# Kernel optimization log

Measured on AMD Instinct MI355X. Metric: run time of the kernel, lower is better.

## Reference

```python
import jax, jax.numpy as jnp
import numpy as np

WINDOW_SIZE = 11
CHANNELS = 3

def _gaussian_window(window_size=WINDOW_SIZE, channels=CHANNELS, sigma=1.5):
    x = np.arange(window_size, dtype=np.float32)
    g = np.exp(-((x - window_size // 2) ** 2) / (2.0 * sigma ** 2))
    g = g / g.sum()
    w2d = np.outer(g, g).astype(np.float32)  # [K,K]
    # depthwise kernel [C, 1, K, K] (OIHW with feature_group_count=C)
    return jnp.asarray(np.broadcast_to(w2d, (channels, 1, window_size, window_size)).copy())

def _depthwise_conv(x, window):
    # x: [B,C,H,W], window: [C,1,K,K]; SAME padding via explicit pad = K//2
    pad = window.shape[-1] // 2
    return jax.lax.conv_general_dilated(
        x, window,
        window_strides=(1, 1),
        padding=[(pad, pad), (pad, pad)],
        dimension_numbers=('NCHW', 'OIHW', 'NCHW'),
        feature_group_count=x.shape[1])

def setup_inputs() -> dict:
    key = jax.random.key(0)
    k1, k2 = jax.random.split(key)
    B, C, H, W = 16, 3, 512, 512
    img1 = jax.random.uniform(k1, (B, C, H, W), dtype=jnp.float32)
    img2 = jax.random.uniform(k2, (B, C, H, W), dtype=jnp.float32)
    window = _gaussian_window()
    return {"img1": img1, "img2": img2, "window": window}

def reference(img1, img2, window):
    eps = 1e-6
    img1 = jnp.clip(img1, eps, 1.0 - eps)
    img2 = jnp.clip(img2, eps, 1.0 - eps)

    mu1 = _depthwise_conv(img1, window)
    mu2 = _depthwise_conv(img2, window)
    mu1_sq = mu1 * mu1
    mu2_sq = mu2 * mu2
    mu1_mu2 = mu1 * mu2

    sigma1_sq = _depthwise_conv(img1 * img1, window) - mu1_sq
    sigma2_sq = _depthwise_conv(img2 * img2, window) - mu2_sq
    sigma12 = _depthwise_conv(img1 * img2, window) - mu1_mu2

    C1 = 0.01 ** 2
    C2 = 0.03 ** 2
    ssim_map = ((2.0 * mu1_mu2 + C1) * (2.0 * sigma12 + C2)) / (
        (mu1_sq + mu2_sq + C1) * (sigma1_sq + sigma2_sq + C2))
    return 1.0 - jnp.mean(ssim_map)
```

## Files before the change

kernel.cpp:

```cpp
#include <hip/hip_runtime.h>

typedef _Float16 f16;
typedef __fp16 fp16x2 __attribute__((ext_vector_type(2)));
typedef _Float16 half4 __attribute__((ext_vector_type(4)));
typedef _Float16 half8 __attribute__((ext_vector_type(8)));
typedef float floatx16 __attribute__((ext_vector_type(16)));

#define FSTR 44
#define XSTR 180
#define WTOT (32 * XSTR)

union H8 { half8 v; half4 h[2]; fp16x2 p[4]; unsigned u[4]; };
union H4 { half4 v; fp16x2 p[2]; };


__device__ __forceinline__ void load_tile(
    const float* __restrict__ img1, const float* __restrict__ img2, size_t base,
    int row, int rowcap, int x0, int q, float4 ra[3][2], float4 rb[3][2], unsigned mk[3])
{
    int rowc = min(max(min(row, rowcap), 0), 511);
    bool rok = (row >= 0) && (row <= 511);
    const float* r1 = img1 + base + (size_t)rowc * 512;
    const float* r2 = img2 + base + (size_t)rowc * 512;
    #pragma unroll
    for (int ch = 0; ch < 3; ++ch) {
        int cb  = x0 - 8 + 16 * ch + 8 * q;
        int cbc = min(max(cb, 0), 504);
        mk[ch] = (cb == cbc && rok) ? 0xFFFFFFFFu : 0u;
        ra[ch][0] = *(const float4*)(r1 + cbc);
        ra[ch][1] = *(const float4*)(r1 + cbc + 4);
        rb[ch][0] = *(const float4*)(r2 + cbc);
        rb[ch][1] = *(const float4*)(r2 + cbc + 4);
    }
}

__device__ __forceinline__ void compute_acct(
    const float4 ra[3][2], const float4 rb[3][2], const unsigned mk[3],
    const half8 band1[3], floatx16 acc[4])
{
    #pragma unroll
    for (int ch = 0; ch < 3; ++ch) {
        H8 F0, F1, F2, F3;
        #pragma unroll
        for (int h = 0; h < 2; ++h) {
            const float as[4] = {ra[ch][h].x, ra[ch][h].y, ra[ch][h].z, ra[ch][h].w};
            const float bs[4] = {rb[ch][h].x, rb[ch][h].y, rb[ch][h].z, rb[ch][h].w};
            #pragma unroll
            for (int t = 0; t < 2; ++t) {
                float a0 = as[2*t], a1 = as[2*t+1];
                float b0 = bs[2*t], b1 = bs[2*t+1];
                int jj = 2 * h + t;
                F0.p[jj] = __builtin_amdgcn_cvt_pkrtz(a0, a1);
                F1.p[jj] = __builtin_amdgcn_cvt_pkrtz(b0, b1);
                F2.p[jj] = __builtin_amdgcn_cvt_pkrtz(a0*a0 + b0*b0, a1*a1 + b1*b1);
                F3.p[jj] = __builtin_amdgcn_cvt_pkrtz(a0*b0, a1*b1);
            }
        }
        unsigned m = mk[ch];
        #pragma unroll
        for (int i = 0; i < 4; ++i) { F0.u[i] &= m; F1.u[i] &= m; F2.u[i] &= m; F3.u[i] &= m; }
        acc[0] = __builtin_amdgcn_mfma_f32_32x32x16_f16(F0.v, band1[ch], acc[0], 0, 0, 0);
        acc[1] = __builtin_amdgcn_mfma_f32_32x32x16_f16(F1.v, band1[ch], acc[1], 0, 0, 0);
        acc[2] = __builtin_amdgcn_mfma_f32_32x32x16_f16(F2.v, band1[ch], acc[2], 0, 0, 0);
        acc[3] = __builtin_amdgcn_mfma_f32_32x32x16_f16(F3.v, band1[ch], acc[3], 0, 0, 0);
    }
}

template<int MT, int FLO, int FHI>
__device__ __forceinline__ void write_T(f16* tx, int q, const floatx16 acc[4])
{
    #pragma unroll
    for (int f = FLO; f < FHI; ++f) {
        #pragma unroll
        for (int s = 0; s < (MT == 0 ? 4 : 2); ++s) {
            const int r0 = 8 * s + 4 * q + 32 * MT;
            H4 h4;
            h4.p[0] = __builtin_amdgcn_cvt_pkrtz(acc[f][4*s],   acc[f][4*s+1]);
            h4.p[1] = __builtin_amdgcn_cvt_pkrtz(acc[f][4*s+2], acc[f][4*s+3]);
            if (MT == 1 && s == 1) {
                if (q == 0) *(half4*)(tx + f * FSTR + r0) = h4.v;
            } else {
                *(half4*)(tx + f * FSTR + r0) = h4.v;
            }
        }
    }
}

__global__ __launch_bounds__(128, 3) void ssim_kernel(
    const float* __restrict__ img1, const float* __restrict__ img2,
    const float* __restrict__ window, float* __restrict__ acc)
{
    __shared__ __align__(16) f16 smem[2 * WTOT];

    const int tid  = threadIdx.x;
    const int lane = tid & 63;
    const int wv   = tid >> 6;
    const int q    = lane >> 5;
    const int ln   = lane & 31;

    const int bz = blockIdx.z;
    const int c  = bz % 3;
    const int x0 = blockIdx.x * 64 + 32 * wv;
    const int oy = blockIdx.y * 32;
    const size_t base = (size_t)bz * (512 * 512);

    f16* Tw = smem + wv * WTOT;

    float4 ra[3][2], rb[3][2]; unsigned mk[3];
    load_tile(img1, img2, base, oy - 5 + ln, 511, x0, q, ra, rb, mk);
    float4 ra1[3][2], rb1[3][2]; unsigned mk1[3];
    load_tile(img1, img2, base, oy + 27 + ln, oy + 36, x0, q, ra1, rb1, mk1);

    float gv = 0.f;
    if (lane < 11) {
        const float* w2 = window + c * 121 + lane * 11;
        #pragma unroll
        for (int j = 0; j < 11; ++j) gv += w2[j];
    }

    if (lane < 32) {
        half4 z4 = {};
        *(half4*)(Tw + lane * XSTR + 176) = z4;
    }

    half8 band1[3], band2[3];
    #pragma unroll
    for (int ch = 0; ch < 3; ++ch) {
        int ib = 16 * ch + 8 * q - ln - 3;
        float gg[11];
        #pragma unroll
        for (int t = 0; t < 11; ++t) gg[t] = __shfl(gv, (ib + t) & 63, 64);
        H8 t1, t2;
        #pragma unroll
        for (int jj = 0; jj < 4; ++jj) {
            fp16x2 p1 = { (__fp16)gg[2*jj],     (__fp16)gg[2*jj + 1] };
            fp16x2 p2 = { (__fp16)gg[2*jj + 3], (__fp16)gg[2*jj + 4] };
            t1.p[jj] = p1; t2.p[jj] = p2;
        }
        band1[ch] = t1.v; band2[ch] = t2.v;
    }

    floatx16 accT[4] = {};
    compute_acct(ra, rb, mk, band1, accT);
    f16* tx = Tw + ln * XSTR;
    write_T<0, 0, 4>(tx, q, accT);

    floatx16 accU[4] = {};
    compute_acct(ra1, rb1, mk1, band1, accU);
    write_T<1, 0, 4>(tx, q, accU);

    floatx16 accH[4] = {};
    #pragma unroll
    for (int ch = 0; ch < 3; ++ch) {
        const f16* tb = Tw + ln * XSTR + 16 * ch + 8 * q;
        #pragma unroll
        for (int f = 0; f < 4; ++f) {
            H8 af;
            af.h[0] = *(const half4*)(tb + f * FSTR);
            af.h[1] = *(const half4*)(tb + f * FSTR + 4);
            accH[f] = __builtin_amdgcn_mfma_f32_32x32x16_f16(af.v, band2[ch], accH[f], 0, 0, 0);
        }
    }

    float vsum = 0.f;
    const float C1 = 1e-4f, C2 = 9e-4f;
    #pragma unroll
    for (int r = 0; r < 16; ++r) {
        float mu1 = accH[0][r], mu2 = accH[1][r];
        float S = accH[2][r], E12 = accH[3][r];
        float mu11 = mu1 * mu1, mu22 = mu2 * mu2, mu12 = mu1 * mu2;
        float num = (2.f * mu12 + C1) * (2.f * (E12 - mu12) + C2);
        float den = (mu11 + mu22 + C1) * (S - mu11 - mu22 + C2);
        vsum += num * __builtin_amdgcn_rcpf(den);
    }

    #pragma unroll
    for (int off = 32; off > 0; off >>= 1) vsum += __shfl_down(vsum, off, 64);
    if (lane == 0) atomicAdd(&acc[bz * 16], vsum);
}

__global__ void ssim_finalize(const float* __restrict__ acc,
                              float* __restrict__ out, float invN)
{
    const int lane = threadIdx.x;
    float v = (lane < 48) ? acc[lane * 16] : 0.f;
    #pragma unroll
    for (int off = 32; off > 0; off >>= 1) v += __shfl_down(v, off, 64);
    if (lane == 0) out[0] = 1.0f - v * invN;
}

extern "C" void kernel_launch(void* const* d_in, const int* in_sizes, int n_in,
                              void* d_out, int out_size, void* d_ws, size_t ws_size,
                              hipStream_t stream) {
    const float* img1 = (const float*)d_in[0];
    const float* img2 = (const float*)d_in[1];
    const float* window = (const float*)d_in[2];
    float* out = (float*)d_out;
    float* acc = (float*)d_ws;

    const float invN = 1.0f / (16.0f * 3.0f * 512.0f * 512.0f);

    hipMemsetAsync(acc, 0, 48 * 16 * sizeof(float), stream);

    dim3 block(128);
    dim3 grid(8, 16, 48);
    ssim_kernel<<<grid, block, 0, stream>>>(img1, img2, window, acc);
    ssim_finalize<<<1, 64, 0, stream>>>(acc, out, invN);
}
```

Before: 146.4 us.

## Keep vertical-pass intermediates in registers via cross-half shuffles instead of LDS

Removes the shared-memory staging of the first MFMA pass results. Accumulator outputs are packed to fp16 in registers and rearranged into the second MFMA's A-operand layout with xor-32 lane shuffles. The second tile load is also deferred until after the first MFMA pass to cut register pressure, and band construction is split into a helper. This drops LDS traffic and capacity in exchange for more DPP/permute shuffles and more live registers.

```diff
diff --git a/kernel.cpp b/kernel.cpp
--- a/kernel.cpp
+++ b/kernel.cpp
@@ -2,17 +2,36 @@
 
 typedef _Float16 f16;
 typedef __fp16 fp16x2 __attribute__((ext_vector_type(2)));
-typedef _Float16 half4 __attribute__((ext_vector_type(4)));
 typedef _Float16 half8 __attribute__((ext_vector_type(8)));
 typedef float floatx16 __attribute__((ext_vector_type(16)));
 
-#define FSTR 44
-#define XSTR 180
-#define WTOT (32 * XSTR)
-
-union H8 { half8 v; half4 h[2]; fp16x2 p[4]; unsigned u[4]; };
-union H4 { half4 v; fp16x2 p[2]; };
-
+union H8 { half8 v; fp16x2 p[4]; unsigned u[4]; };
+union P2 { fp16x2 p; unsigned u; };
+
+
+__device__ __forceinline__ unsigned pk(float a, float b) {
+    P2 t; t.p = __builtin_amdgcn_cvt_pkrtz(a, b); return t.u;
+}
+
+__device__ __forceinline__ void halfswap(bool lo, unsigned a, unsigned b,
+                                         unsigned &r0, unsigned &r1) {
+    unsigned as = (unsigned)__shfl_xor((int)a, 32, 64);
+    unsigned bs = (unsigned)__shfl_xor((int)b, 32, 64);
+    r0 = lo ? a  : bs;
+    r1 = lo ? as : b;
+}
+
+__device__ __forceinline__ half8 mkband(float gv, int ib) {
+    H8 t;
+    #pragma unroll
+    for (int jj = 0; jj < 4; ++jj) {
+        float g0 = __shfl(gv, (ib + 2 * jj)     & 63, 64);
+        float g1 = __shfl(gv, (ib + 2 * jj + 1) & 63, 64);
+        fp16x2 pp = { (__fp16)g0, (__fp16)g1 };
+        t.p[jj] = pp;
+    }
+    return t.v;
+}
 
 __device__ __forceinline__ void load_tile(
     const float* __restrict__ img1, const float* __restrict__ img2, size_t base,
@@ -66,37 +85,16 @@
     }
 }
 
-template<int MT, int FLO, int FHI>
-__device__ __forceinline__ void write_T(f16* tx, int q, const floatx16 acc[4])
-{
-    #pragma unroll
-    for (int f = FLO; f < FHI; ++f) {
-        #pragma unroll
-        for (int s = 0; s < (MT == 0 ? 4 : 2); ++s) {
-            const int r0 = 8 * s + 4 * q + 32 * MT;
-            H4 h4;
-            h4.p[0] = __builtin_amdgcn_cvt_pkrtz(acc[f][4*s],   acc[f][4*s+1]);
-            h4.p[1] = __builtin_amdgcn_cvt_pkrtz(acc[f][4*s+2], acc[f][4*s+3]);
-            if (MT == 1 && s == 1) {
-                if (q == 0) *(half4*)(tx + f * FSTR + r0) = h4.v;
-            } else {
-                *(half4*)(tx + f * FSTR + r0) = h4.v;
-            }
-        }
-    }
-}
-
 __global__ __launch_bounds__(128, 3) void ssim_kernel(
     const float* __restrict__ img1, const float* __restrict__ img2,
     const float* __restrict__ window, float* __restrict__ acc)
 {
-    __shared__ __align__(16) f16 smem[2 * WTOT];
-
     const int tid  = threadIdx.x;
     const int lane = tid & 63;
     const int wv   = tid >> 6;
     const int q    = lane >> 5;
     const int ln   = lane & 31;
+    const bool lo  = (q == 0);
 
     const int bz = blockIdx.z;
     const int c  = bz % 3;
@@ -104,12 +102,8 @@
     const int oy = blockIdx.y * 32;
     const size_t base = (size_t)bz * (512 * 512);
 
-    f16* Tw = smem + wv * WTOT;
-
     float4 ra[3][2], rb[3][2]; unsigned mk[3];
     load_tile(img1, img2, base, oy - 5 + ln, 511, x0, q, ra, rb, mk);
-    float4 ra1[3][2], rb1[3][2]; unsigned mk1[3];
-    load_tile(img1, img2, base, oy + 27 + ln, oy + 36, x0, q, ra1, rb1, mk1);
 
     float gv = 0.f;
     if (lane < 11) {
@@ -118,47 +112,55 @@
         for (int j = 0; j < 11; ++j) gv += w2[j];
     }
 
-    if (lane < 32) {
-        half4 z4 = {};
-        *(half4*)(Tw + lane * XSTR + 176) = z4;
-    }
-
-    half8 band1[3], band2[3];
-    #pragma unroll
-    for (int ch = 0; ch < 3; ++ch) {
-        int ib = 16 * ch + 8 * q - ln - 3;
-        float gg[11];
-        #pragma unroll
-        for (int t = 0; t < 11; ++t) gg[t] = __shfl(gv, (ib + t) & 63, 64);
-        H8 t1, t2;
-        #pragma unroll
-        for (int jj = 0; jj < 4; ++jj) {
-            fp16x2 p1 = { (__fp16)gg[2*jj],     (__fp16)gg[2*jj + 1] };
-            fp16x2 p2 = { (__fp16)gg[2*jj + 3], (__fp16)gg[2*jj + 4] };
-            t1.p[jj] = p1; t2.p[jj] = p2;
-        }
-        band1[ch] = t1.v; band2[ch] = t2.v;
-    }
+    half8 band1[3];
+    #pragma unroll
+    for (int ch = 0; ch < 3; ++ch) band1[ch] = mkband(gv, 16 * ch + 8 * q - ln - 3);
 
     floatx16 accT[4] = {};
     compute_acct(ra, rb, mk, band1, accT);
-    f16* tx = Tw + ln * XSTR;
-    write_T<0, 0, 4>(tx, q, accT);
+
+    float4 ra1[3][2], rb1[3][2]; unsigned mk1[3];
+    load_tile(img1, img2, base, oy + 27 + ln, oy + 36, x0, q, ra1, rb1, mk1);
+
+    unsigned cT[4][4][2];
+    #pragma unroll
+    for (int f = 0; f < 4; ++f)
+        #pragma unroll
+        for (int s = 0; s < 4; ++s)
+            #pragma unroll
+            for (int i = 0; i < 2; ++i)
+                cT[f][s][i] = pk(accT[f][4*s + 2*i], accT[f][4*s + 2*i + 1]);
 
     floatx16 accU[4] = {};
     compute_acct(ra1, rb1, mk1, band1, accU);
-    write_T<1, 0, 4>(tx, q, accU);
+
+    unsigned cU[4][2][2];
+    #pragma unroll
+    for (int f = 0; f < 4; ++f)
+        #pragma unroll
+        for (int s = 0; s < 2; ++s)
+            #pragma unroll
+            for (int i = 0; i < 2; ++i)
+                cU[f][s][i] = pk(accU[f][4*s + 2*i], accU[f][4*s + 2*i + 1]);
+
+    half8 band2[3];
+    #pragma unroll
+    for (int ch = 0; ch < 3; ++ch) band2[ch] = mkband(gv, 16 * ch + 8 * q - ln);
 
     floatx16 accH[4] = {};
     #pragma unroll
-    for (int ch = 0; ch < 3; ++ch) {
-        const f16* tb = Tw + ln * XSTR + 16 * ch + 8 * q;
+    for (int kb = 0; kb < 3; ++kb) {
         #pragma unroll
         for (int f = 0; f < 4; ++f) {
-            H8 af;
-            af.h[0] = *(const half4*)(tb + f * FSTR);
-            af.h[1] = *(const half4*)(tb + f * FSTR + 4);
-            accH[f] = __builtin_amdgcn_mfma_f32_32x32x16_f16(af.v, band2[ch], accH[f], 0, 0, 0);
+            unsigned a0 = (kb < 2) ? cT[f][2*kb][0]     : cU[f][0][0];
+            unsigned b0 = (kb < 2) ? cT[f][2*kb + 1][0] : cU[f][1][0];
+            unsigned a1 = (kb < 2) ? cT[f][2*kb][1]     : cU[f][0][1];
+            unsigned b1 = (kb < 2) ? cT[f][2*kb + 1][1] : cU[f][1][1];
+            unsigned d0, d1, d2, d3;
+            halfswap(lo, a0, b0, d0, d2);
+            halfswap(lo, a1, b1, d1, d3);
+            H8 A; A.u[0] = d0; A.u[1] = d1; A.u[2] = d2; A.u[3] = d3;
+            accH[f] = __builtin_amdgcn_mfma_f32_32x32x16_f16(A.v, band2[kb], accH[f], 0, 0, 0);
         }
     }
 
```

After: 157.8 us. 1.08x slower.

## Remap block order across XCDs and defer second band construction

Applied to the files above, without the earlier changes.

Blocks get a new linear-id mapping: consecutive hardware block ids, which the hardware spreads round-robin across the XCDs, now land on contiguous tiles so each XCD works on neighbouring image regions and shares halo rows in its own L2. The second band matrix is now built after the first pass rather than up front, through a helper that shuffles only the 8 needed weights. This shortens register live ranges, which matters under the 3-blocks-per-SM launch bound. The remap assumes 8 XCDs and the exact 6144-block grid.

```diff
diff --git a/kernel.cpp b/kernel.cpp
--- a/kernel.cpp
+++ b/kernel.cpp
@@ -86,6 +86,18 @@
     }
 }
 
+__device__ __forceinline__ half8 mkband(float gv, int ib) {
+    H8 t;
+    #pragma unroll
+    for (int jj = 0; jj < 4; ++jj) {
+        float g0 = __shfl(gv, (ib + 2 * jj)     & 63, 64);
+        float g1 = __shfl(gv, (ib + 2 * jj + 1) & 63, 64);
+        fp16x2 pp = { (__fp16)g0, (__fp16)g1 };
+        t.p[jj] = pp;
+    }
+    return t.v;
+}
+
 __global__ __launch_bounds__(128, 3) void ssim_kernel(
     const float* __restrict__ img1, const float* __restrict__ img2,
     const float* __restrict__ window, float* __restrict__ acc)
@@ -98,10 +110,15 @@
     const int q    = lane >> 5;
     const int ln   = lane & 31;
 
-    const int bz = blockIdx.z;
+    const int orig = blockIdx.x + 8 * blockIdx.y + 128 * blockIdx.z;
+    const int nid  = (orig & 7) * 768 + (orig >> 3);
+    const int bx = nid & 7;
+    const int by = (nid >> 3) & 15;
+    const int bz = nid >> 7;
+
     const int c  = bz % 3;
-    const int x0 = blockIdx.x * 64 + 32 * wv;
-    const int oy = blockIdx.y * 32;
+    const int x0 = bx * 64 + 32 * wv;
+    const int oy = by * 32;
     const size_t base = (size_t)bz * (512 * 512);
 
     f16* Tw = smem + wv * WTOT;
@@ -123,22 +140,9 @@
         *(half4*)(Tw + lane * XSTR + 176) = z4;
     }
 
-    half8 band1[3], band2[3];
-    #pragma unroll
-    for (int ch = 0; ch < 3; ++ch) {
-        int ib = 16 * ch + 8 * q - ln - 3;
-        float gg[11];
-        #pragma unroll
-        for (int t = 0; t < 11; ++t) gg[t] = __shfl(gv, (ib + t) & 63, 64);
-        H8 t1, t2;
-        #pragma unroll
-        for (int jj = 0; jj < 4; ++jj) {
-            fp16x2 p1 = { (__fp16)gg[2*jj],     (__fp16)gg[2*jj + 1] };
-            fp16x2 p2 = { (__fp16)gg[2*jj + 3], (__fp16)gg[2*jj + 4] };
-            t1.p[jj] = p1; t2.p[jj] = p2;
-        }
-        band1[ch] = t1.v; band2[ch] = t2.v;
-    }
+    half8 band1[3];
+    #pragma unroll
+    for (int ch = 0; ch < 3; ++ch) band1[ch] = mkband(gv, 16 * ch + 8 * q - ln - 3);
 
     floatx16 accT[4] = {};
     compute_acct(ra, rb, mk, band1, accT);
@@ -148,6 +152,10 @@
     floatx16 accU[4] = {};
     compute_acct(ra1, rb1, mk1, band1, accU);
     write_T<1, 0, 4>(tx, q, accU);
+
+    half8 band2[3];
+    #pragma unroll
+    for (int ch = 0; ch < 3; ++ch) band2[ch] = mkband(gv, 16 * ch + 8 * q - ln);
 
     floatx16 accH[4] = {};
     #pragma unroll
```

Result: slower. 152.4 us (+4.2%).
